# Kernel optimization log

Hardware: AMD Instinct MI355X
Metric: run time of the kernel (lower is better)

The kernel has to match this reference:

```python
import jax, jax.numpy as jnp
import numpy as np

RES = 8          # voxel_resolution
CLASSES = 40
B, N = 64, 100000


def setup_inputs() -> dict:
    key = jax.random.key(0)
    kx, kw, kb = jax.random.split(key, 3)
    x = jax.random.normal(kx, (B, N, 3), dtype=jnp.float32)
    f = RES ** 3
    # nn.Linear(f, CLASSES): W is (out, in), uniform(-1/sqrt(in), 1/sqrt(in))
    bound = 1.0 / np.sqrt(f)
    W = jax.random.uniform(kw, (CLASSES, f), dtype=jnp.float32, minval=-bound, maxval=bound)
    b = jax.random.uniform(kb, (CLASSES,), dtype=jnp.float32, minval=-bound, maxval=bound)
    return {"x": x, "W": W, "b": b}


def _count_points(x):
    # x: (B, N, 3) -> per-batch adaptive-range 3D histogram, normalized by N
    b_, n_, _ = x.shape
    mins = x.min(axis=1, keepdims=True)            # (B,1,3)
    maxs = x.max(axis=1, keepdims=True)            # (B,1,3)
    rng = maxs - mins
    scale = RES / jnp.where(rng > 0, rng, 1.0)
    # bin index per point per dim; points at max fall in last bin (histogramdd
    # right-closes the final bin) -> clip to RES-1
    idx = jnp.clip(jnp.floor((x - mins) * scale).astype(jnp.int32), 0, RES - 1)  # (B,N,3)
    flat = (idx[..., 0] * RES + idx[..., 1]) * RES + idx[..., 2]                 # (B,N)
    flat = flat + (jnp.arange(b_, dtype=jnp.int32) * (RES ** 3))[:, None]
    counts = jax.ops.segment_sum(
        jnp.ones((b_ * n_,), dtype=x.dtype),
        flat.reshape(-1),
        num_segments=b_ * RES ** 3,
    ).reshape(b_, RES ** 3)
    return counts / n_


def reference(x, W, b):
    counts = _count_points(x)           # (B, RES^3), mode='count'
    logits = counts @ W.T + b           # (B, CLASSES)
    return logits
```

## Files before the change

### kernel.cpp

```cpp
#include <hip/hip_runtime.h>
#include <hip/hip_cooperative_groups.h>

namespace cg = cooperative_groups;

#define RES 8
#define F 512
#define CLASSES 40
#define B 64
#define NPTS 100000
#define NSLOT (NPTS / 4)

#define BLKS 16
#define TPB (BLKS * 256)
#define NFULL 6
#define TAILCUT (NSLOT - NFULL * TPB)

#define PARTH_OFF 0
#define PARTMM_OFF (B * BLKS * F)
#define CNT_OFF (PARTMM_OFF + B * BLKS * 6)

#define MM4(pA, pB, pC) do { \
    m0 = fminf(m0, fminf(fminf((pA).x, (pA).w), fminf((pB).z, (pC).y))); \
    M0 = fmaxf(M0, fmaxf(fmaxf((pA).x, (pA).w), fmaxf((pB).z, (pC).y))); \
    m1 = fminf(m1, fminf(fminf((pA).y, (pB).x), fminf((pB).w, (pC).z))); \
    M1 = fmaxf(M1, fmaxf(fmaxf((pA).y, (pB).x), fmaxf((pB).w, (pC).z))); \
    m2 = fminf(m2, fminf(fminf((pA).z, (pB).y), fminf((pC).x, (pC).w))); \
    M2 = fmaxf(M2, fmaxf(fmaxf((pA).z, (pB).y), fmaxf((pC).x, (pC).w))); \
} while (0)

#define BIN1(X, Y, Z) do { \
    int i0 = (int)floorf(((X) - mn0) * sc0); \
    int i1 = (int)floorf(((Y) - mn1) * sc1); \
    int i2 = (int)floorf(((Z) - mn2) * sc2); \
    i0 = min(max(i0, 0), RES - 1); \
    i1 = min(max(i1, 0), RES - 1); \
    i2 = min(max(i2, 0), RES - 1); \
    atomicAdd(&myh[(i0 * RES + i1) * RES + i2], 1u); \
} while (0)

#define BIN4(pA, pB, pC) do { \
    BIN1((pA).x, (pA).y, (pA).z); \
    BIN1((pA).w, (pB).x, (pB).y); \
    BIN1((pB).z, (pB).w, (pC).x); \
    BIN1((pC).y, (pC).z, (pC).w); \
} while (0)

__global__ __launch_bounds__(256, 4) void fused_kernel(const float* __restrict__ x,
                                                       const float* __restrict__ Wm,
                                                       const float* __restrict__ bias,
                                                       float* __restrict__ out,
                                                       unsigned int* __restrict__ ws) {
    const int sub   = blockIdx.x;
    const int batch = blockIdx.y;
    const int t     = threadIdx.x;

    __shared__ unsigned int lh[4][F];
    __shared__ float red[6][BLKS];
    __shared__ float smn[3], ssc[3];
    __shared__ float wmin[4][3], wmax[4][3];
    __shared__ float cf[F];
    __shared__ int swin;

    for (int i = t; i < 4 * F; i += 256) ((unsigned int*)lh)[i] = 0u;

    if (sub == 0 && t == 0)
        __hip_atomic_store(&ws[CNT_OFF + batch * 16], 0u,
                           __ATOMIC_RELAXED, __HIP_MEMORY_SCOPE_AGENT);

    const float4* xb4 = (const float4*)(x + (size_t)batch * (NPTS * 3));
    const int g = sub * 256 + t;
    const float4* bp = xb4 + 3 * g;
    const bool tail = (g < TAILCUT);

    float4 c0a = bp[0],         c0b = bp[1],         c0c = bp[2];
    float4 c1a = bp[12288],     c1b = bp[12289],     c1c = bp[12290];
    float4 c2a = bp[24576],     c2b = bp[24577],     c2c = bp[24578];
    float4 c3a = bp[36864],     c3b = bp[36865],     c3c = bp[36866];
    float4 c4a = bp[49152],     c4b = bp[49153],     c4c = bp[49154];
    float4 c5a = bp[61440],     c5b = bp[61441],     c5c = bp[61442];

    {
        float m0 = 3.0e38f, m1 = 3.0e38f, m2 = 3.0e38f;
        float M0 = -3.0e38f, M1 = -3.0e38f, M2 = -3.0e38f;
        MM4(c0a, c0b, c0c);
        MM4(c1a, c1b, c1c);
        MM4(c2a, c2b, c2c);
        MM4(c3a, c3b, c3c);
        MM4(c4a, c4b, c4c);
        MM4(c5a, c5b, c5c);
        if (tail) {
            float4 ta = bp[73728], tb = bp[73729], tc = bp[73730];
            MM4(ta, tb, tc);
        }
        for (int d = 1; d < 64; d <<= 1) {
            m0 = fminf(m0, __shfl_xor(m0, d)); M0 = fmaxf(M0, __shfl_xor(M0, d));
            m1 = fminf(m1, __shfl_xor(m1, d)); M1 = fmaxf(M1, __shfl_xor(M1, d));
            m2 = fminf(m2, __shfl_xor(m2, d)); M2 = fmaxf(M2, __shfl_xor(M2, d));
        }
        const int wave = t >> 6;
        if ((t & 63) == 0) {
            wmin[wave][0] = m0; wmin[wave][1] = m1; wmin[wave][2] = m2;
            wmax[wave][0] = M0; wmax[wave][1] = M1; wmax[wave][2] = M2;
        }
        __syncthreads();
        if (t < 3) {
            float mn = fminf(fminf(wmin[0][t], wmin[1][t]), fminf(wmin[2][t], wmin[3][t]));
            float mx = fmaxf(fmaxf(wmax[0][t], wmax[1][t]), fmaxf(wmax[2][t], wmax[3][t]));
            float* pm = (float*)(ws + PARTMM_OFF) + ((size_t)batch * BLKS + sub) * 6;
            pm[t]     = mn;
            pm[3 + t] = mx;
        }
    }

    cg::this_grid().sync();

    {
        const float* pm = (const float*)(ws + PARTMM_OFF) + (size_t)batch * BLKS * 6;
        if (t < 6 * BLKS) {
            const int c = t % 6, j = t / 6;
            red[c][j] = pm[j * 6 + c];
        }
        __syncthreads();
        if (t < 3) {
            float mn = red[t][0], mx = red[t + 3][0];
#pragma unroll
            for (int j = 1; j < BLKS; ++j) {
                mn = fminf(mn, red[t][j]);
                mx = fmaxf(mx, red[t + 3][j]);
            }
            float rng = mx - mn;
            smn[t] = mn;
            ssc[t] = (float)RES / (rng > 0.0f ? rng : 1.0f);
        }
        __syncthreads();
    }

    {
        const float mn0 = smn[0], mn1 = smn[1], mn2 = smn[2];
        const float sc0 = ssc[0], sc1 = ssc[1], sc2 = ssc[2];
        unsigned int* myh = lh[t >> 6];

        BIN4(c0a, c0b, c0c);
        BIN4(c1a, c1b, c1c);
        BIN4(c2a, c2b, c2c);
        BIN4(c3a, c3b, c3c);
        BIN4(c4a, c4b, c4c);
        BIN4(c5a, c5b, c5c);
        if (tail) {
            float4 ta = bp[73728], tb = bp[73729], tc = bp[73730];
            BIN4(ta, tb, tc);
        }
        __syncthreads();

        unsigned int* ph = ws + PARTH_OFF + ((size_t)batch * BLKS + sub) * F;
        for (int bin = t; bin < F; bin += 256)
            ph[bin] = lh[0][bin] + lh[1][bin] + lh[2][bin] + lh[3][bin];
        __syncthreads();
    }

    if (t == 0) {
        __threadfence();
        unsigned int old = __hip_atomic_fetch_add(&ws[CNT_OFF + batch * 16], 1u,
                                                  __ATOMIC_ACQ_REL,
                                                  __HIP_MEMORY_SCOPE_AGENT);
        swin = (old == BLKS - 1);
    }
    __syncthreads();
    if (!swin) return;
    __threadfence();

    {
        const unsigned int* ph = ws + PARTH_OFF + (size_t)batch * BLKS * F;
        for (int bin = t; bin < F; bin += 256) {
            unsigned int s = 0;
#pragma unroll
            for (int j = 0; j < BLKS; ++j) s += ph[j * F + bin];
            cf[bin] = (float)s * (1.0f / (float)NPTS);
        }
        __syncthreads();
        if (t < CLASSES) {
            const float4* wr  = (const float4*)(Wm + t * F);
            const float4* cf4 = (const float4*)cf;
            float d0 = 0.f, d1 = 0.f, d2 = 0.f, d3 = 0.f;
#pragma unroll 4
            for (int k = 0; k < F / 4; k += 4) {
                float4 w0 = wr[k],   c0 = cf4[k];
                float4 w1 = wr[k+1], c1 = cf4[k+1];
                float4 w2 = wr[k+2], c2 = cf4[k+2];
                float4 w3 = wr[k+3], c3 = cf4[k+3];
                d0 += c0.x*w0.x + c0.y*w0.y + c0.z*w0.z + c0.w*w0.w;
                d1 += c1.x*w1.x + c1.y*w1.y + c1.z*w1.z + c1.w*w1.w;
                d2 += c2.x*w2.x + c2.y*w2.y + c2.z*w2.z + c2.w*w2.w;
                d3 += c3.x*w3.x + c3.y*w3.y + c3.z*w3.z + c3.w*w3.w;
            }
            out[batch * CLASSES + t] = ((d0 + d1) + (d2 + d3)) + bias[t];
        }
    }
}

__global__ __launch_bounds__(256) void minmax_kernel(const float* __restrict__ x,
                                                     unsigned int* __restrict__ ws) {
    const int sub = blockIdx.x, batch = blockIdx.y, t = threadIdx.x;
    const float4* xb4 = (const float4*)(x + (size_t)batch * (NPTS * 3));
    float m0 = 3.0e38f, m1 = 3.0e38f, m2 = 3.0e38f;
    float M0 = -3.0e38f, M1 = -3.0e38f, M2 = -3.0e38f;
    for (int i = sub * 256 + t; i < NSLOT; i += BLKS * 256) {
        float4 pA = xb4[3 * i + 0];
        float4 pB = xb4[3 * i + 1];
        float4 pC = xb4[3 * i + 2];
        MM4(pA, pB, pC);
    }
    for (int d = 1; d < 64; d <<= 1) {
        m0 = fminf(m0, __shfl_xor(m0, d)); M0 = fmaxf(M0, __shfl_xor(M0, d));
        m1 = fminf(m1, __shfl_xor(m1, d)); M1 = fmaxf(M1, __shfl_xor(M1, d));
        m2 = fminf(m2, __shfl_xor(m2, d)); M2 = fmaxf(M2, __shfl_xor(M2, d));
    }
    __shared__ float wmin[4][3], wmax[4][3];
    const int wave = t >> 6;
    if ((t & 63) == 0) {
        wmin[wave][0] = m0; wmin[wave][1] = m1; wmin[wave][2] = m2;
        wmax[wave][0] = M0; wmax[wave][1] = M1; wmax[wave][2] = M2;
    }
    __syncthreads();
    if (t < 3) {
        float mn = fminf(fminf(wmin[0][t], wmin[1][t]), fminf(wmin[2][t], wmin[3][t]));
        float mx = fmaxf(fmaxf(wmax[0][t], wmax[1][t]), fmaxf(wmax[2][t], wmax[3][t]));
        float* pm = (float*)(ws + PARTMM_OFF) + ((size_t)batch * BLKS + sub) * 6;
        pm[t] = mn;
        pm[3 + t] = mx;
    }
}

__global__ __launch_bounds__(256) void hist_kernel(const float* __restrict__ x,
                                                   unsigned int* __restrict__ ws) {
    const int sub = blockIdx.x, batch = blockIdx.y, t = threadIdx.x;
    __shared__ unsigned int lh[4][F];
    __shared__ float red[6][BLKS];
    __shared__ float smn[3], ssc[3];
    for (int i = t; i < 4 * F; i += 256) ((unsigned int*)lh)[i] = 0u;

    const float* pm = (const float*)(ws + PARTMM_OFF) + (size_t)batch * BLKS * 6;
    if (t < 6 * BLKS) {
        const int c = t % 6, j = t / 6;
        red[c][j] = pm[j * 6 + c];
    }
    __syncthreads();
    if (t < 3) {
        float mn = red[t][0], mx = red[t + 3][0];
#pragma unroll
        for (int j = 1; j < BLKS; ++j) {
            mn = fminf(mn, red[t][j]);
            mx = fmaxf(mx, red[t + 3][j]);
        }
        float rng = mx - mn;
        smn[t] = mn;
        ssc[t] = (float)RES / (rng > 0.0f ? rng : 1.0f);
    }
    __syncthreads();

    const float mn0 = smn[0], mn1 = smn[1], mn2 = smn[2];
    const float sc0 = ssc[0], sc1 = ssc[1], sc2 = ssc[2];
    const float4* xb4 = (const float4*)(x + (size_t)batch * (NPTS * 3));
    unsigned int* myh = lh[t >> 6];
    for (int i = sub * 256 + t; i < NSLOT; i += BLKS * 256) {
        float4 pA = xb4[3 * i + 0];
        float4 pB = xb4[3 * i + 1];
        float4 pC = xb4[3 * i + 2];
        BIN4(pA, pB, pC);
    }
    __syncthreads();
    unsigned int* ph = ws + PARTH_OFF + ((size_t)batch * BLKS + sub) * F;
    for (int bin = t; bin < F; bin += 256)
        ph[bin] = lh[0][bin] + lh[1][bin] + lh[2][bin] + lh[3][bin];
}

__global__ __launch_bounds__(256) void logits_kernel(const unsigned int* __restrict__ ws,
                                                     const float* __restrict__ Wm,
                                                     const float* __restrict__ bias,
                                                     float* __restrict__ out) {
    const int batch = blockIdx.x, t = threadIdx.x;
    __shared__ float cf[F];
    const unsigned int* ph = ws + PARTH_OFF + (size_t)batch * BLKS * F;
    for (int bin = t; bin < F; bin += 256) {
        unsigned int s = 0;
#pragma unroll
        for (int j = 0; j < BLKS; ++j) s += ph[j * F + bin];
        cf[bin] = (float)s * (1.0f / (float)NPTS);
    }
    __syncthreads();
    if (t < CLASSES) {
        const float4* wr  = (const float4*)(Wm + t * F);
        const float4* cf4 = (const float4*)cf;
        float d0 = 0.f, d1 = 0.f, d2 = 0.f, d3 = 0.f;
#pragma unroll 4
        for (int k = 0; k < F / 4; k += 4) {
            float4 w0 = wr[k],   c0 = cf4[k];
            float4 w1 = wr[k+1], c1 = cf4[k+1];
            float4 w2 = wr[k+2], c2 = cf4[k+2];
            float4 w3 = wr[k+3], c3 = cf4[k+3];
            d0 += c0.x*w0.x + c0.y*w0.y + c0.z*w0.z + c0.w*w0.w;
            d1 += c1.x*w1.x + c1.y*w1.y + c1.z*w1.z + c1.w*w1.w;
            d2 += c2.x*w2.x + c2.y*w2.y + c2.z*w2.z + c2.w*w2.w;
            d3 += c3.x*w3.x + c3.y*w3.y + c3.z*w3.z + c3.w*w3.w;
        }
        out[batch * CLASSES + t] = ((d0 + d1) + (d2 + d3)) + bias[t];
    }
}

extern "C" void kernel_launch(void* const* d_in, const int* in_sizes, int n_in,
                              void* d_out, int out_size, void* d_ws, size_t ws_size,
                              hipStream_t stream) {
    const float* x    = (const float*)d_in[0];
    const float* Wm   = (const float*)d_in[1];
    const float* bias = (const float*)d_in[2];
    float* out        = (float*)d_out;
    unsigned int* ws  = (unsigned int*)d_ws;

    static int coop_ok = -1;
    if (coop_ok < 0) {
        int dev = 0;
        hipGetDevice(&dev);
        hipDeviceProp_t prop{};
        hipGetDeviceProperties(&prop, dev);
        int nb = 0;
        hipError_t e = hipOccupancyMaxActiveBlocksPerMultiprocessor(
            &nb, (const void*)fused_kernel, 256, 0);
        coop_ok = (e == hipSuccess && prop.cooperativeLaunch &&
                   (long)nb * prop.multiProcessorCount >= (long)BLKS * B) ? 1 : 0;
    }

    if (coop_ok) {
        void* args[] = {(void*)&x, (void*)&Wm, (void*)&bias, (void*)&out, (void*)&ws};
        hipLaunchCooperativeKernel((const void*)fused_kernel, dim3(BLKS, B), dim3(256),
                                   args, 0, stream);
    } else {
        minmax_kernel<<<dim3(BLKS, B), 256, 0, stream>>>(x, ws);
        hist_kernel<<<dim3(BLKS, B), 256, 0, stream>>>(x, ws);
        logits_kernel<<<B, 256, 0, stream>>>(ws, Wm, bias, out);
    }
}
```

Measured before the change: 126.6 us.

## Double blocks per batch, reload points from memory, split logits dot across threads

Doubles the blocks per batch from 16 to 32 and raises the occupancy hint to 8, so each thread handles 3 point slots instead of 6. Points are no longer held in registers between the min/max pass and the binning pass; they are reloaded from global memory (likely from cache) so the lower register budget fits. The final logits dot product is spread over 4 threads per class with a shared-memory reduction to shorten the single-block tail. The risks are the second read of the input, a larger cooperative grid that must still be co-resident, and more partial histograms to sum at the end.

```diff
diff --git a/kernel.cpp b/kernel.cpp
--- a/kernel.cpp
+++ b/kernel.cpp
@@ -10,9 +10,9 @@
 #define NPTS 100000
 #define NSLOT (NPTS / 4)
 
-#define BLKS 16
+#define BLKS 32
 #define TPB (BLKS * 256)
-#define NFULL 6
+#define NFULL 3
 #define TAILCUT (NSLOT - NFULL * TPB)
 
 #define PARTH_OFF 0
@@ -45,7 +45,7 @@
     BIN1((pC).y, (pC).z, (pC).w); \
 } while (0)
 
-__global__ __launch_bounds__(256, 4) void fused_kernel(const float* __restrict__ x,
+__global__ __launch_bounds__(256, 8) void fused_kernel(const float* __restrict__ x,
                                                        const float* __restrict__ Wm,
                                                        const float* __restrict__ bias,
                                                        float* __restrict__ out,
@@ -59,38 +59,35 @@
     __shared__ float smn[3], ssc[3];
     __shared__ float wmin[4][3], wmax[4][3];
     __shared__ float cf[F];
+    __shared__ float part[CLASSES][4];
     __shared__ int swin;
 
     for (int i = t; i < 4 * F; i += 256) ((unsigned int*)lh)[i] = 0u;
 
     if (sub == 0 && t == 0)
-        __hip_atomic_store(&ws[CNT_OFF + batch * 16], 0u,
-                           __ATOMIC_RELAXED, __HIP_MEMORY_SCOPE_AGENT);
+        ws[CNT_OFF + batch * 16] = 0u;
 
     const float4* xb4 = (const float4*)(x + (size_t)batch * (NPTS * 3));
     const int g = sub * 256 + t;
-    const float4* bp = xb4 + 3 * g;
     const bool tail = (g < TAILCUT);
-
-    float4 c0a = bp[0],         c0b = bp[1],         c0c = bp[2];
-    float4 c1a = bp[12288],     c1b = bp[12289],     c1c = bp[12290];
-    float4 c2a = bp[24576],     c2b = bp[24577],     c2c = bp[24578];
-    float4 c3a = bp[36864],     c3b = bp[36865],     c3c = bp[36866];
-    float4 c4a = bp[49152],     c4b = bp[49153],     c4c = bp[49154];
-    float4 c5a = bp[61440],     c5b = bp[61441],     c5c = bp[61442];
 
     {
         float m0 = 3.0e38f, m1 = 3.0e38f, m2 = 3.0e38f;
         float M0 = -3.0e38f, M1 = -3.0e38f, M2 = -3.0e38f;
-        MM4(c0a, c0b, c0c);
-        MM4(c1a, c1b, c1c);
-        MM4(c2a, c2b, c2c);
-        MM4(c3a, c3b, c3c);
-        MM4(c4a, c4b, c4c);
-        MM4(c5a, c5b, c5c);
+#pragma unroll
+        for (int k = 0; k < NFULL; ++k) {
+            const int i = g + k * TPB;
+            float4 pA = xb4[3 * i + 0];
+            float4 pB = xb4[3 * i + 1];
+            float4 pC = xb4[3 * i + 2];
+            MM4(pA, pB, pC);
+        }
         if (tail) {
-            float4 ta = bp[73728], tb = bp[73729], tc = bp[73730];
-            MM4(ta, tb, tc);
+            const int i = g + NFULL * TPB;
+            float4 pA = xb4[3 * i + 0];
+            float4 pB = xb4[3 * i + 1];
+            float4 pC = xb4[3 * i + 2];
+            MM4(pA, pB, pC);
         }
         for (int d = 1; d < 64; d <<= 1) {
             m0 = fminf(m0, __shfl_xor(m0, d)); M0 = fmaxf(M0, __shfl_xor(M0, d));
@@ -139,16 +136,20 @@
         const float mn0 = smn[0], mn1 = smn[1], mn2 = smn[2];
         const float sc0 = ssc[0], sc1 = ssc[1], sc2 = ssc[2];
         unsigned int* myh = lh[t >> 6];
-
-        BIN4(c0a, c0b, c0c);
-        BIN4(c1a, c1b, c1c);
-        BIN4(c2a, c2b, c2c);
-        BIN4(c3a, c3b, c3c);
-        BIN4(c4a, c4b, c4c);
-        BIN4(c5a, c5b, c5c);
+#pragma unroll
+        for (int k = 0; k < NFULL; ++k) {
+            const int i = g + k * TPB;
+            float4 pA = xb4[3 * i + 0];
+            float4 pB = xb4[3 * i + 1];
+            float4 pC = xb4[3 * i + 2];
+            BIN4(pA, pB, pC);
+        }
         if (tail) {
-            float4 ta = bp[73728], tb = bp[73729], tc = bp[73730];
-            BIN4(ta, tb, tc);
+            const int i = g + NFULL * TPB;
+            float4 pA = xb4[3 * i + 0];
+            float4 pB = xb4[3 * i + 1];
+            float4 pC = xb4[3 * i + 2];
+            BIN4(pA, pB, pC);
         }
         __syncthreads();
 
@@ -170,20 +171,21 @@
     __threadfence();
 
     {
-        const unsigned int* ph = ws + PARTH_OFF + (size_t)batch * BLKS * F;
+        const unsigned int* php = ws + PARTH_OFF + (size_t)batch * BLKS * F;
         for (int bin = t; bin < F; bin += 256) {
             unsigned int s = 0;
 #pragma unroll
-            for (int j = 0; j < BLKS; ++j) s += ph[j * F + bin];
+            for (int j = 0; j < BLKS; ++j) s += php[j * F + bin];
             cf[bin] = (float)s * (1.0f / (float)NPTS);
         }
         __syncthreads();
-        if (t < CLASSES) {
-            const float4* wr  = (const float4*)(Wm + t * F);
-            const float4* cf4 = (const float4*)cf;
+        if (t < CLASSES * 4) {
+            const int c = t >> 2, q = t & 3;
+            const float4* wr  = (const float4*)(Wm + c * F) + q * 32;
+            const float4* cf4 = (const float4*)cf + q * 32;
             float d0 = 0.f, d1 = 0.f, d2 = 0.f, d3 = 0.f;
 #pragma unroll 4
-            for (int k = 0; k < F / 4; k += 4) {
+            for (int k = 0; k < 32; k += 4) {
                 float4 w0 = wr[k],   c0 = cf4[k];
                 float4 w1 = wr[k+1], c1 = cf4[k+1];
                 float4 w2 = wr[k+2], c2 = cf4[k+2];
@@ -193,8 +195,12 @@
                 d2 += c2.x*w2.x + c2.y*w2.y + c2.z*w2.z + c2.w*w2.w;
                 d3 += c3.x*w3.x + c3.y*w3.y + c3.z*w3.z + c3.w*w3.w;
             }
-            out[batch * CLASSES + t] = ((d0 + d1) + (d2 + d3)) + bias[t];
-        }
+            part[c][q] = ((d0 + d1) + (d2 + d3));
+        }
+        __syncthreads();
+        if (t < CLASSES)
+            out[batch * CLASSES + t] =
+                ((part[t][0] + part[t][1]) + (part[t][2] + part[t][3])) + bias[t];
     }
 }
 
@@ -280,6 +286,7 @@
                                                      float* __restrict__ out) {
     const int batch = blockIdx.x, t = threadIdx.x;
     __shared__ float cf[F];
+    __shared__ float part[CLASSES][4];
     const unsigned int* ph = ws + PARTH_OFF + (size_t)batch * BLKS * F;
     for (int bin = t; bin < F; bin += 256) {
         unsigned int s = 0;
@@ -288,12 +295,13 @@
         cf[bin] = (float)s * (1.0f / (float)NPTS);
     }
     __syncthreads();
-    if (t < CLASSES) {
-        const float4* wr  = (const float4*)(Wm + t * F);
-        const float4* cf4 = (const float4*)cf;
+    if (t < CLASSES * 4) {
+        const int c = t >> 2, q = t & 3;
+        const float4* wr  = (const float4*)(Wm + c * F) + q * 32;
+        const float4* cf4 = (const float4*)cf + q * 32;
         float d0 = 0.f, d1 = 0.f, d2 = 0.f, d3 = 0.f;
 #pragma unroll 4
-        for (int k = 0; k < F / 4; k += 4) {
+        for (int k = 0; k < 32; k += 4) {
             float4 w0 = wr[k],   c0 = cf4[k];
             float4 w1 = wr[k+1], c1 = cf4[k+1];
             float4 w2 = wr[k+2], c2 = cf4[k+2];
@@ -303,8 +311,12 @@
             d2 += c2.x*w2.x + c2.y*w2.y + c2.z*w2.z + c2.w*w2.w;
             d3 += c3.x*w3.x + c3.y*w3.y + c3.z*w3.z + c3.w*w3.w;
         }
-        out[batch * CLASSES + t] = ((d0 + d1) + (d2 + d3)) + bias[t];
-    }
+        part[c][q] = ((d0 + d1) + (d2 + d3));
+    }
+    __syncthreads();
+    if (t < CLASSES)
+        out[batch * CLASSES + t] =
+            ((part[t][0] + part[t][1]) + (part[t][2] + part[t][3])) + bias[t];
 }
 
 extern "C" void kernel_launch(void* const* d_in, const int* in_sizes, int n_in,
```

New measurement: 127.8 us. About the same (+1.0%).
